# Performance work log

Measured on AMD Instinct MI355X. Metric: run time of the kernel, lower is better.

Reference implementation:

```python
import jax, jax.numpy as jnp
import numpy as np

EPS = 1e-12

def _ff_degree(x, w_in, scale, bias, w_out):
    # x: [b, n, d, m]; w_in: [d, h]; scale/bias: [1, 1, h]; w_out: [h, d]
    h = jnp.einsum('bndm,dh->bnhm', x, w_in)
    norm = jnp.clip(jnp.linalg.norm(h, axis=-1, keepdims=True), EPS, None)  # [b,n,h,1]
    phase = h / norm
    gated = jax.nn.gelu(norm[..., 0] * scale + bias, approximate=False)[..., None]
    h = gated * phase
    return jnp.einsum('bnhm,hd->bndm', h, w_out)


def setup_inputs() -> dict:
    key = jax.random.key(0)
    ks = jax.random.split(key, 16)
    b, n, dim, mult = 4, 4096, 256, 4
    hid = dim * mult
    degrees = [0, 1, 2]
    inp = {}
    for i, deg in enumerate(degrees):
        m = 2 * deg + 1
        inp[f'x{deg}'] = jax.random.normal(ks[i], (b, n, dim, m), dtype=jnp.float32)
        inp[f'w_in{deg}'] = jax.random.normal(ks[3 + i], (dim, hid), dtype=jnp.float32) / np.sqrt(dim)
        inp[f'scale{deg}'] = jnp.ones((1, 1, hid), dtype=jnp.float32)
        inp[f'bias{deg}'] = jax.random.uniform(ks[6 + i], (1, 1, hid), dtype=jnp.float32, minval=-0.001, maxval=0.001)
        inp[f'w_out{deg}'] = jax.random.normal(ks[9 + i], (hid, dim), dtype=jnp.float32) / np.sqrt(hid)
    return inp


def reference(x0, x1, x2,
              w_in0, scale0, bias0, w_out0,
              w_in1, scale1, bias1, w_out1,
              w_in2, scale2, bias2, w_out2):
    y0 = _ff_degree(x0, w_in0, scale0, bias0, w_out0)
    y1 = _ff_degree(x1, w_in1, scale1, bias1, w_out1)
    y2 = _ff_degree(x2, w_in2, scale2, bias2, w_out2)
    return (y0, y1, y2)
```

## Files before the change

kernel.cpp:

```cpp
#include <hip/hip_runtime.h>
#include <hip/hip_bf16.h>


typedef __attribute__((ext_vector_type(8))) short short8;
typedef __attribute__((ext_vector_type(4))) float f32x4;

static __device__ __forceinline__ short f2bf(float f) {
  __hip_bfloat16 h = __float2bfloat16(f);
  return *reinterpret_cast<short*>(&h);
}

__global__ void pack_all_k(const float* __restrict__ w0i, const float* __restrict__ w0o,
                           const float* __restrict__ w1i, const float* __restrict__ w1o,
                           const float* __restrict__ w2i, const float* __restrict__ w2o,
                           short* __restrict__ p) {
  const int region = blockIdx.x >> 7;
  const int gid = (blockIdx.x & 127) * 256 + threadIdx.x;
  const int lane = gid & 63;
  const int tile = gid >> 6;
  const int gg = lane >> 4, cc = lane & 15;
  const float* w = (region == 0) ? w0i : (region == 1) ? w0o :
                   (region == 2) ? w1i : (region == 3) ? w1o :
                   (region == 4) ? w2i : w2o;
  short8 v;
  if (region & 1) {
    const int nt2 = tile & 15, kt2 = tile >> 4;
#pragma unroll
    for (int j = 0; j < 8; ++j)
      v[j] = f2bf(w[(kt2 * 32 + gg * 8 + j) * 256 + nt2 * 16 + cc]);
  } else {
    const int kt = tile & 7, nt = tile >> 3;
#pragma unroll
    for (int j = 0; j < 8; ++j)
      v[j] = f2bf(w[(kt * 32 + gg * 8 + j) * 1024 + nt * 16 + cc]);
  }
  *reinterpret_cast<short8*>(p + ((size_t)region * 262144) + gid * 8) = v;
}

template<int NT, int GRP, int OUT_M>
__global__ __launch_bounds__(512, 4)
void ff_se3_kernel(const float* __restrict__ x,
                   const short* __restrict__ wpin,
                   const short* __restrict__ wpout,
                   const float* __restrict__ scale,
                   const float* __restrict__ bias,
                   float* __restrict__ out)
{
  constexpr int T = 16 * NT;
  constexpr int R = (OUT_M == 1) ? T : 16;
  extern __shared__ short lds[];
  short* lA  = lds;
  short* lH0 = lds + T * 256;
  short* lH1 = lH0 + T * 128;

  const int tid  = threadIdx.x;
  const int lane = tid & 63;
  const int wave = tid >> 6;
  const int g    = lane >> 4;
  const int lc   = lane & 15;
  const long row0 = (long)blockIdx.x * R;

  for (int e4 = tid; e4 < R * 64 * OUT_M; e4 += 512) {
    const int r  = e4 / (64 * OUT_M);
    const int o4 = e4 - r * (64 * OUT_M);
    const f32x4 v = __builtin_nontemporal_load(
        reinterpret_cast<const f32x4*>(x + (row0 + r) * (256 * OUT_M) + o4 * 4));
#pragma unroll
    for (int i = 0; i < 4; ++i) {
      const int flat = o4 * 4 + i;
      const int d  = flat / OUT_M;
      const int mm = flat - d * OUT_M;
      const int t  = mm * 16 + r;
      const int byte = t * 512 + ((d * 2) ^ ((t & 7) << 4));
      lA[byte >> 1] = f2bf(v[i]);
    }
  }

  f32x4 acc_out[NT][2];
#pragma unroll
  for (int a = 0; a < NT; ++a) { acc_out[a][0] = (f32x4)(0.f); acc_out[a][1] = (f32x4)(0.f); }

  __syncthreads();

  for (int c = 0; c < 8; ++c) {
    short* lH = (c & 1) ? lH1 : lH0;

    const int hgl = c * 128 + wave * 16 + lc;
    const float sc = scale[hgl];
    const float bi = bias[hgl];

    f32x4 acc1[NT];
#pragma unroll
    for (int a = 0; a < NT; ++a) acc1[a] = (f32x4)(0.f);
#pragma unroll
    for (int kt = 0; kt < 8; ++kt) {
      short8 af[NT];
#pragma unroll
      for (int a = 0; a < NT; ++a) {
        const int t = a * 16 + lc;
        const int byte = t * 512 + (((kt * 32 + g * 8) * 2) ^ ((t & 7) << 4));
        af[a] = *reinterpret_cast<const short8*>(&lA[byte >> 1]);
      }
      const int ntg = c * 8 + wave;
      const short8 bfr = *reinterpret_cast<const short8*>(wpin + ((ntg * 8 + kt) * 64 + lane) * 8);
#pragma unroll
      for (int a = 0; a < NT; ++a)
        acc1[a] = __builtin_amdgcn_mfma_f32_16x16x32_bf16(af[a], bfr, acc1[a], 0, 0, 0);
    }

    short8 b2p[4][2];
#pragma unroll
    for (int kk = 0; kk < 4; ++kk)
#pragma unroll
      for (int nn = 0; nn < 2; ++nn) {
        const int tile = (c * 4 + kk) * 16 + wave * 2 + nn;
        b2p[kk][nn] = *reinterpret_cast<const short8*>(wpout + (tile * 64 + lane) * 8);
      }

#pragma unroll
    for (int reg = 0; reg < 4; ++reg) {
#pragma unroll
      for (int gi = 0; gi < NT / GRP; ++gi) {
        float ns = 0.f;
#pragma unroll
        for (int k = 0; k < GRP; ++k) {
          const float h = acc1[gi * GRP + k][reg];
          ns += h * h;
        }
        ns = fmaxf(ns, 1e-24f);
        const float rn  = __builtin_amdgcn_rsqf(ns);
        const float nrm = ns * rn;
        const float z   = fmaf(nrm, sc, bi);
        float u2 = 2.f * z * fmaf(0.0356774081f * z, z, 0.7978845608f);
        u2 = fminf(u2, 30.f);
        const float e  = __expf(u2);
        const float th = (e - 1.f) * __builtin_amdgcn_rcpf(e + 1.f);
        const float fac = 0.5f * (1.f + th) * z * rn;
        const int tl  = g * 4 + reg;
        const int col = wave * 16 + lc;
#pragma unroll
        for (int k = 0; k < GRP; ++k) {
          const int a = gi * GRP + k;
          const int t = a * 16 + tl;
          const int byte = t * 256 + ((col * 2) ^ ((t & 7) << 4));
          lH[byte >> 1] = f2bf(acc1[a][reg] * fac);
        }
      }
    }

    __syncthreads();

#pragma unroll
    for (int kk = 0; kk < 4; ++kk) {
      short8 a2[NT];
#pragma unroll
      for (int a = 0; a < NT; ++a) {
        const int t = a * 16 + lc;
        const int byte = t * 256 + (((kk * 32 + g * 8) * 2) ^ ((t & 7) << 4));
        a2[a] = *reinterpret_cast<const short8*>(&lH[byte >> 1]);
      }
#pragma unroll
      for (int a = 0; a < NT; ++a)
#pragma unroll
        for (int nn = 0; nn < 2; ++nn)
          acc_out[a][nn] = __builtin_amdgcn_mfma_f32_16x16x32_bf16(a2[a], b2p[kk][nn], acc_out[a][nn], 0, 0, 0);
    }
  }

  __syncthreads();
  float* ldsF = reinterpret_cast<float*>(lds);
  constexpr int RW = 256 * OUT_M;
  if constexpr (OUT_M == 1) {
#pragma unroll
    for (int a = 0; a < NT; ++a)
#pragma unroll
      for (int nn = 0; nn < 2; ++nn) {
        const int d = wave * 32 + nn * 16 + lc;
#pragma unroll
        for (int reg = 0; reg < 4; ++reg) {
          const int t = a * 16 + g * 4 + reg;
          ldsF[t * RW + d] = acc_out[a][nn][reg];
        }
      }
  } else {
#pragma unroll
    for (int mm = 0; mm < NT; ++mm)
#pragma unroll
      for (int nn = 0; nn < 2; ++nn) {
        const int d = wave * 32 + nn * 16 + lc;
#pragma unroll
        for (int reg = 0; reg < 4; ++reg) {
          const int r = g * 4 + reg;
          ldsF[r * RW + d * OUT_M + mm] = acc_out[mm][nn][reg];
        }
      }
  }
  __syncthreads();
  float* obase = out + row0 * RW;
  constexpr int NF4 = (R * RW) / 4;
  for (int i = tid; i < NF4; i += 512) {
    const f32x4 v = *reinterpret_cast<const f32x4*>(&ldsF[i * 4]);
    __builtin_nontemporal_store(v, reinterpret_cast<f32x4*>(obase) + i);
  }
}

extern "C" void kernel_launch(void* const* d_in, const int* in_sizes, int n_in,
                              void* d_out, int out_size, void* d_ws, size_t ws_size,
                              hipStream_t stream)
{
  short* ws = (short*)d_ws;
  const size_t WSZ = 262144;
  float* outf = (float*)d_out;
  const size_t out_off[3] = {0, 4194304, 16777216};

  pack_all_k<<<768, 256, 0, stream>>>(
      (const float*)d_in[1],  (const float*)d_in[4],
      (const float*)d_in[6],  (const float*)d_in[9],
      (const float*)d_in[11], (const float*)d_in[14], ws);

  for (int dg = 0; dg < 3; ++dg) {
    const float* x  = (const float*)d_in[5 * dg + 0];
    const float* sc = (const float*)d_in[5 * dg + 2];
    const float* bi = (const float*)d_in[5 * dg + 3];
    const short* pin  = ws + (2 * dg) * WSZ;
    const short* pout = ws + (2 * dg + 1) * WSZ;
    float* o = outf + out_off[dg];
    switch (dg) {
      case 0:
        ff_se3_kernel<2, 1, 1><<<512, 512, 32768, stream>>>(x, pin, pout, sc, bi, o);
        break;
      case 1:
        ff_se3_kernel<3, 3, 3><<<1024, 512, 49152, stream>>>(x, pin, pout, sc, bi, o);
        break;
      case 2:
        ff_se3_kernel<5, 5, 5><<<1024, 512, 81920, stream>>>(x, pin, pout, sc, bi, o);
        break;
    }
  }
}
```

Measured before the change: 231.6 us.

## Pre-pack activations into MFMA fragment layout and read A operands from global

```diff
diff --git a/kernel.cpp b/kernel.cpp
--- a/kernel.cpp
+++ b/kernel.cpp
@@ -37,9 +37,47 @@
   *reinterpret_cast<short8*>(p + ((size_t)region * 262144) + gid * 8) = v;
 }
 
-template<int NT, int GRP, int OUT_M>
+__global__ __launch_bounds__(256)
+void pack_x_k(const float* __restrict__ x1, const float* __restrict__ x2,
+              short* __restrict__ xf1, short* __restrict__ xf2) {
+  const bool d2 = blockIdx.x >= 1024;
+  const int rb = d2 ? (blockIdx.x - 1024) : blockIdx.x;
+  const int M  = d2 ? 5 : 3;
+  const float* x = d2 ? x2 : x1;
+  short* xf = d2 ? xf2 : xf1;
+  extern __shared__ short sA[];
+  const int tid = threadIdx.x, lane = tid & 63, wave = tid >> 6;
+  const int g = lane >> 4, lc = lane & 15;
+
+  for (int e4 = tid; e4 < 16 * 64 * M; e4 += 256) {
+    const int r  = e4 / (64 * M);
+    const int o4 = e4 - r * (64 * M);
+    const f32x4 v = __builtin_nontemporal_load(
+        reinterpret_cast<const f32x4*>(x + ((size_t)rb * 16 + r) * (256 * M) + o4 * 4));
+#pragma unroll
+    for (int i = 0; i < 4; ++i) {
+      const int flat = o4 * 4 + i;
+      const int d  = flat / M;
+      const int mm = flat - d * M;
+      const int t  = mm * 16 + r;
+      const int byte = t * 512 + ((d * 2) ^ ((t & 7) << 4));
+      sA[byte >> 1] = f2bf(v[i]);
+    }
+  }
+  __syncthreads();
+  for (int idx = wave; idx < M * 8; idx += 4) {
+    const int mm = idx >> 3, kt = idx & 7;
+    const int t = mm * 16 + lc;
+    const int byte = t * 512 + (((kt * 32 + g * 8) * 2) ^ ((t & 7) << 4));
+    const short8 f = *reinterpret_cast<const short8*>(&sA[byte >> 1]);
+    *reinterpret_cast<short8*>(xf + ((((size_t)rb * M + mm) * 8 + kt) * 64 + lane) * 8) = f;
+  }
+}
+
+template<int NT, int GRP, int OUT_M, int MODE>
 __global__ __launch_bounds__(512, 4)
 void ff_se3_kernel(const float* __restrict__ x,
+                   const short* __restrict__ xfrag,
                    const short* __restrict__ wpin,
                    const short* __restrict__ wpout,
                    const float* __restrict__ scale,
@@ -50,7 +88,7 @@
   constexpr int R = (OUT_M == 1) ? T : 16;
   extern __shared__ short lds[];
   short* lA  = lds;
-  short* lH0 = lds + T * 256;
+  short* lH0 = (MODE == 0) ? (lds + T * 256) : lds;
   short* lH1 = lH0 + T * 128;
 
   const int tid  = threadIdx.x;
@@ -60,19 +98,21 @@
   const int lc   = lane & 15;
   const long row0 = (long)blockIdx.x * R;
 
-  for (int e4 = tid; e4 < R * 64 * OUT_M; e4 += 512) {
-    const int r  = e4 / (64 * OUT_M);
-    const int o4 = e4 - r * (64 * OUT_M);
-    const f32x4 v = __builtin_nontemporal_load(
-        reinterpret_cast<const f32x4*>(x + (row0 + r) * (256 * OUT_M) + o4 * 4));
-#pragma unroll
-    for (int i = 0; i < 4; ++i) {
-      const int flat = o4 * 4 + i;
-      const int d  = flat / OUT_M;
-      const int mm = flat - d * OUT_M;
-      const int t  = mm * 16 + r;
-      const int byte = t * 512 + ((d * 2) ^ ((t & 7) << 4));
-      lA[byte >> 1] = f2bf(v[i]);
+  if constexpr (MODE == 0) {
+    for (int e4 = tid; e4 < R * 64 * OUT_M; e4 += 512) {
+      const int r  = e4 / (64 * OUT_M);
+      const int o4 = e4 - r * (64 * OUT_M);
+      const f32x4 v = __builtin_nontemporal_load(
+          reinterpret_cast<const f32x4*>(x + (row0 + r) * (256 * OUT_M) + o4 * 4));
+#pragma unroll
+      for (int i = 0; i < 4; ++i) {
+        const int flat = o4 * 4 + i;
+        const int d  = flat / OUT_M;
+        const int mm = flat - d * OUT_M;
+        const int t  = mm * 16 + r;
+        const int byte = t * 512 + ((d * 2) ^ ((t & 7) << 4));
+        lA[byte >> 1] = f2bf(v[i]);
+      }
     }
   }
 
@@ -80,7 +120,7 @@
 #pragma unroll
   for (int a = 0; a < NT; ++a) { acc_out[a][0] = (f32x4)(0.f); acc_out[a][1] = (f32x4)(0.f); }
 
-  __syncthreads();
+  if constexpr (MODE == 0) __syncthreads();
 
   for (int c = 0; c < 8; ++c) {
     short* lH = (c & 1) ? lH1 : lH0;
@@ -97,9 +137,22 @@
       short8 af[NT];
 #pragma unroll
       for (int a = 0; a < NT; ++a) {
-        const int t = a * 16 + lc;
-        const int byte = t * 512 + (((kt * 32 + g * 8) * 2) ^ ((t & 7) << 4));
-        af[a] = *reinterpret_cast<const short8*>(&lA[byte >> 1]);
+        if constexpr (MODE == 0) {
+          const int t = a * 16 + lc;
+          const int byte = t * 512 + (((kt * 32 + g * 8) * 2) ^ ((t & 7) << 4));
+          af[a] = *reinterpret_cast<const short8*>(&lA[byte >> 1]);
+        } else if constexpr (MODE == 1) {
+          af[a] = *reinterpret_cast<const short8*>(
+              xfrag + ((((size_t)blockIdx.x * NT + a) * 8 + kt) * 64 + lane) * 8);
+        } else {
+          const float* xp = x + (((size_t)blockIdx.x * 32 + a * 16 + lc) * 256 + kt * 32 + g * 8);
+          const f32x4 p0 = *reinterpret_cast<const f32x4*>(xp);
+          const f32x4 p1 = *reinterpret_cast<const f32x4*>(xp + 4);
+          short8 t8;
+#pragma unroll
+          for (int j = 0; j < 4; ++j) { t8[j] = f2bf(p0[j]); t8[4 + j] = f2bf(p1[j]); }
+          af[a] = t8;
+        }
       }
       const int ntg = c * 8 + wave;
       const short8 bfr = *reinterpret_cast<const short8*>(wpin + ((ntg * 8 + kt) * 64 + lane) * 8);
@@ -142,7 +195,7 @@
         for (int k = 0; k < GRP; ++k) {
           const int a = gi * GRP + k;
           const int t = a * 16 + tl;
-          const int byte = t * 256 + ((col * 2) ^ ((t & 7) << 4));
+          const int byte = t * 256 + ((col * 2) ^ ((t & 15) << 4));
           lH[byte >> 1] = f2bf(acc1[a][reg] * fac);
         }
       }
@@ -156,7 +209,7 @@
 #pragma unroll
       for (int a = 0; a < NT; ++a) {
         const int t = a * 16 + lc;
-        const int byte = t * 256 + (((kk * 32 + g * 8) * 2) ^ ((t & 7) << 4));
+        const int byte = t * 256 + (((kk * 32 + g * 8) * 2) ^ ((t & 15) << 4));
         a2[a] = *reinterpret_cast<const short8*>(&lH[byte >> 1]);
       }
 #pragma unroll
@@ -210,31 +263,45 @@
 {
   short* ws = (short*)d_ws;
   const size_t WSZ = 262144;
+  short* xf1 = ws + 6 * WSZ;
+  short* xf2 = xf1 + (size_t)1024 * 3 * 8 * 512;
+  const size_t need_bytes =
+      (6 * WSZ + (size_t)1024 * 3 * 8 * 512 + (size_t)1024 * 5 * 8 * 512) * 2;
+  const bool gaf = (ws_size >= need_bytes);
+
   float* outf = (float*)d_out;
   const size_t out_off[3] = {0, 4194304, 16777216};
+
+  const float* x0 = (const float*)d_in[0];
+  const float* x1 = (const float*)d_in[5];
+  const float* x2 = (const float*)d_in[10];
 
   pack_all_k<<<768, 256, 0, stream>>>(
       (const float*)d_in[1],  (const float*)d_in[4],
       (const float*)d_in[6],  (const float*)d_in[9],
       (const float*)d_in[11], (const float*)d_in[14], ws);
-
-  for (int dg = 0; dg < 3; ++dg) {
-    const float* x  = (const float*)d_in[5 * dg + 0];
-    const float* sc = (const float*)d_in[5 * dg + 2];
-    const float* bi = (const float*)d_in[5 * dg + 3];
-    const short* pin  = ws + (2 * dg) * WSZ;
-    const short* pout = ws + (2 * dg + 1) * WSZ;
-    float* o = outf + out_off[dg];
-    switch (dg) {
-      case 0:
-        ff_se3_kernel<2, 1, 1><<<512, 512, 32768, stream>>>(x, pin, pout, sc, bi, o);
-        break;
-      case 1:
-        ff_se3_kernel<3, 3, 3><<<1024, 512, 49152, stream>>>(x, pin, pout, sc, bi, o);
-        break;
-      case 2:
-        ff_se3_kernel<5, 5, 5><<<1024, 512, 81920, stream>>>(x, pin, pout, sc, bi, o);
-        break;
-    }
-  }
-}
+  if (gaf)
+    pack_x_k<<<2048, 256, 40960, stream>>>(x1, x2, xf1, xf2);
+
+  ff_se3_kernel<2, 1, 1, 2><<<512, 512, 32768, stream>>>(
+      x0, nullptr, ws + 0 * WSZ, ws + 1 * WSZ,
+      (const float*)d_in[2], (const float*)d_in[3], outf + out_off[0]);
+
+  if (gaf)
+    ff_se3_kernel<3, 3, 3, 1><<<1024, 512, 49152, stream>>>(
+        x1, xf1, ws + 2 * WSZ, ws + 3 * WSZ,
+        (const float*)d_in[7], (const float*)d_in[8], outf + out_off[1]);
+  else
+    ff_se3_kernel<3, 3, 3, 0><<<1024, 512, 49152, stream>>>(
+        x1, nullptr, ws + 2 * WSZ, ws + 3 * WSZ,
+        (const float*)d_in[7], (const float*)d_in[8], outf + out_off[1]);
+
+  if (gaf)
+    ff_se3_kernel<5, 5, 5, 1><<<1024, 512, 81920, stream>>>(
+        x2, xf2, ws + 4 * WSZ, ws + 5 * WSZ,
+        (const float*)d_in[12], (const float*)d_in[13], outf + out_off[2]);
+  else
+    ff_se3_kernel<5, 5, 5, 0><<<1024, 512, 81920, stream>>>(
+        x2, nullptr, ws + 4 * WSZ, ws + 5 * WSZ,
+        (const float*)d_in[12], (const float*)d_in[13], outf + out_off[2]);
+}
```

After: 817.4 us. 3.53x slower.
